# Kernel tuning notes

Hardware: AMD Instinct MI355X
Metric: run time of the kernel (lower is better)

The kernel has to match this reference:

```python
import jax, jax.numpy as jnp
import numpy as np

N = 100000       # nodes
E = 1600000      # edges per graph
D_IN, D_H, D_OUT = 256, 64, 32
TEM = (0.9, 0.8)  # tem[0], tem[1]


def setup_inputs() -> dict:
    key = jax.random.key(0)
    ks = jax.random.split(key, 17)
    f32 = jnp.float32
    return {
        "features": jax.random.normal(ks[0], (N, D_IN), f32),
        # GraphConv layer1: glorot-ish weight [in, out] + bias
        "W1": jax.random.normal(ks[1], (D_IN, D_H), f32) / np.sqrt(D_IN).astype(np.float32),
        "b1": jnp.zeros((D_H,), f32),
        "W2": jax.random.normal(ks[2], (D_H, D_OUT), f32) / np.sqrt(D_H).astype(np.float32),
        "b2": jnp.zeros((D_OUT,), f32),
        # gating linears: nn.Linear(2*d, 1) -> weight [1, 2*d], bias [1]
        "ga11_w": jax.random.normal(ks[3], (1, 2 * D_H), f32) * 0.1,
        "ga11_b": jnp.zeros((1,), f32),
        "ga12_w": jax.random.normal(ks[4], (1, 2 * D_H), f32) * 0.1,
        "ga12_b": jnp.zeros((1,), f32),
        "ga21_w": jax.random.normal(ks[5], (1, 2 * D_OUT), f32) * 0.1,
        "ga21_b": jnp.zeros((1,), f32),
        "ga22_w": jax.random.normal(ks[6], (1, 2 * D_OUT), f32) * 0.1,
        "ga22_b": jnp.zeros((1,), f32),
        # two graphs as edge lists over the same N nodes
        "src1": jax.random.randint(ks[7], (E,), 0, N, jnp.int32),
        "dst1": jax.random.randint(ks[8], (E,), 0, N, jnp.int32),
        "src2": jax.random.randint(ks[9], (E,), 0, N, jnp.int32),
        "dst2": jax.random.randint(ks[10], (E,), 0, N, jnp.int32),
    }


def _graph_conv(feat, W, b, src, dst):
    """DGL GraphConv, norm='both': D_dst^{-1/2} A^T D_src^{-1/2} X W + b.
    in_feats > out_feats for both layers, so W is applied before aggregation."""
    ones = jnp.ones(src.shape[0], feat.dtype)
    deg_out = jnp.clip(jax.ops.segment_sum(ones, src, num_segments=N), 1.0)  # [N]
    deg_in = jnp.clip(jax.ops.segment_sum(ones, dst, num_segments=N), 1.0)   # [N]
    h = (feat * jax.lax.rsqrt(deg_out)[:, None]) @ W                          # [N, d_out]
    agg = jax.ops.segment_sum(h[src], dst, num_segments=N)                    # SpMM scatter-add
    return agg * jax.lax.rsqrt(deg_in)[:, None] + b


def _gate(xa, xb, w, b, tem):
    """Faithful to: ga = softmax(Linear(cat[xa,xb]), dim=1); diag(ga) -> ga[0,0];
    xb' = tem * diag * xb. softmax over a size-1 axis gives ones; dropout is a
    no-op in eval mode."""
    ga = jnp.concatenate([xa, xb], axis=1) @ w.T + b  # [N, 1]
    ga = jax.nn.softmax(ga, axis=1)                   # all ones ([N,1], axis of size 1)
    d = ga[0, 0]                                      # torch.diag of [N,1] -> scalar ga[0,0]
    return tem * d * xb


def reference(features, W1, b1, W2, b2, ga11_w, ga11_b, ga12_w, ga12_b,
              ga21_w, ga21_b, ga22_w, ga22_b, src1, dst1, src2, dst2):
    x11 = _graph_conv(features, W1, b1, src1, dst1)
    x12 = _graph_conv(features, W1, b1, src2, dst2)
    x12 = _gate(x11, x12, ga11_w, ga11_b, TEM[1])
    x11 = _gate(x12, x11, ga12_w, ga12_b, TEM[0])
    x1 = x11 + x12
    x21 = _graph_conv(x1, W2, b2, src1, dst1)
    x22 = _graph_conv(x1, W2, b2, src2, dst2)
    x22 = _gate(x21, x22, ga21_w, ga21_b, TEM[1])
    x21 = _gate(x22, x21, ga22_w, ga22_b, TEM[0])
    return x21 + x22
```

## Files before the change

kernel.cpp:

```cpp
#include <hip/hip_runtime.h>
#include <hip/hip_bf16.h>

#define TEM0 0.9f
#define TEM1 0.8f
#define NPB 256
#define CAP 4608
#define CHUNKE 2048
#define MAXBUCK 512

typedef __attribute__((ext_vector_type(8))) short bf16x8;
typedef __attribute__((ext_vector_type(4))) float f32x4;

static __device__ __forceinline__ short f2bf(float x) {
  union { __hip_bfloat16 h; short s; } u;
  u.h = __float2bfloat16(x);
  return u.s;
}
static __device__ __forceinline__ float bf2f(short s) {
  union { float f; unsigned u; } v;
  v.u = ((unsigned)(unsigned short)s) << 16;
  return v.f;
}

__global__ __launch_bounds__(256) void bucket_gemm(
    const int* __restrict__ src1, const int* __restrict__ dst1,
    const int* __restrict__ src2, const int* __restrict__ dst2,
    int* gcur_d, int* gcur_s,
    int* __restrict__ rawD1, int* __restrict__ rawD2,
    unsigned char* __restrict__ rawS1, unsigned char* __restrict__ rawS2,
    int E, int NCH, int NBUCK,
    const float* __restrict__ X, const short* __restrict__ Wb,
    short* __restrict__ Yb, int n)
{
  __shared__ int sd[CHUNKE];
  __shared__ int ss[CHUNKE];
  __shared__ int outD[CHUNKE];
  __shared__ int hist[MAXBUCK], strt[MAXBUCK], cur[MAXBUCK], basz[MAXBUCK];
  __shared__ int tmp[256];
  __shared__ short bucketOf[CHUNKE];

  if ((int)blockIdx.x < 2 * NCH) {
    int g = 0, cb = blockIdx.x;
    if (cb >= NCH) { g = 1; cb -= NCH; }
    const int* src = g ? src2 : src1;
    const int* dst = g ? dst2 : dst1;
    int* rawD = g ? rawD2 : rawD1;
    unsigned char* rawS = g ? rawS2 : rawS1;
    int* curD = gcur_d + g * NBUCK;
    int* curS = gcur_s + g * NBUCK;
    int tid = threadIdx.x;
    int e0 = cb * CHUNKE;
    int K = min(CHUNKE, E - e0);

    for (int i = tid; i < K; i += 256) { sd[i] = dst[e0 + i]; ss[i] = src[e0 + i]; }
    hist[tid] = 0; hist[tid + 256] = 0;
    __syncthreads();

    for (int i = tid; i < K; i += 256) atomicAdd(&hist[sd[i] >> 8], 1);
    __syncthreads();
    int h0 = hist[2 * tid], h1 = hist[2 * tid + 1];
    tmp[tid] = h0 + h1;
    __syncthreads();
    for (int off = 1; off < 256; off <<= 1) {
      int t = (tid >= off) ? tmp[tid - off] : 0;
      __syncthreads();
      tmp[tid] += t;
      __syncthreads();
    }
    int ep = tmp[tid] - (h0 + h1);
    strt[2 * tid] = ep; strt[2 * tid + 1] = ep + h0;
    cur[2 * tid] = 0;  cur[2 * tid + 1] = 0;
    __syncthreads();
    for (int b = tid; b < NBUCK; b += 256) {
      int c = hist[b];
      basz[b] = c ? atomicAdd(&curD[b], c) : 0;
      int st = strt[b];
      for (int j = 0; j < c; ++j) bucketOf[st + j] = (short)b;
    }
    __syncthreads();
    for (int i = tid; i < K; i += 256) {
      int d = sd[i];
      int b = d >> 8;
      int p = atomicAdd(&cur[b], 1);
      outD[strt[b] + p] = ((d & 255) << 17) | ss[i];
    }
    __syncthreads();
    for (int i = tid; i < K; i += 256) {
      int b = bucketOf[i];
      int off = basz[b] + (i - strt[b]);
      if (off < CAP) rawD[(size_t)b * CAP + off] = outD[i];
    }

    __syncthreads();
    hist[tid] = 0; hist[tid + 256] = 0;
    __syncthreads();
    for (int i = tid; i < K; i += 256) atomicAdd(&hist[ss[i] >> 8], 1);
    __syncthreads();
    h0 = hist[2 * tid]; h1 = hist[2 * tid + 1];
    tmp[tid] = h0 + h1;
    __syncthreads();
    for (int off = 1; off < 256; off <<= 1) {
      int t = (tid >= off) ? tmp[tid - off] : 0;
      __syncthreads();
      tmp[tid] += t;
      __syncthreads();
    }
    ep = tmp[tid] - (h0 + h1);
    strt[2 * tid] = ep; strt[2 * tid + 1] = ep + h0;
    cur[2 * tid] = 0;  cur[2 * tid + 1] = 0;
    __syncthreads();
    for (int b = tid; b < NBUCK; b += 256) {
      int c = hist[b];
      basz[b] = c ? atomicAdd(&curS[b], c) : 0;
      int st = strt[b];
      for (int j = 0; j < c; ++j) bucketOf[st + j] = (short)b;
    }
    __syncthreads();
    unsigned char* outS = (unsigned char*)outD;
    for (int i = tid; i < K; i += 256) {
      int s = ss[i];
      int b = s >> 8;
      int p = atomicAdd(&cur[b], 1);
      outS[strt[b] + p] = (unsigned char)(s & 255);
    }
    __syncthreads();
    for (int i = tid; i < K; i += 256) {
      int b = bucketOf[i];
      int off = basz[b] + (i - strt[b]);
      if (off < CAP) rawS[(size_t)b * CAP + off] = outS[i];
    }
  } else {
    int bid = (int)blockIdx.x - 2 * NCH;
    int w = threadIdx.x >> 6;
    int l = threadIdx.x & 63;
    int row = bid * 64 + w * 16 + (l & 15);
    int rowc = row < n ? row : n - 1;
    int ko = (l >> 4) << 3;

    f32x4 acc[4] = {};
    const float* xrow = X + (size_t)rowc * 256;

#pragma unroll
    for (int kk = 0; kk < 8; ++kk) {
      const float4* p = reinterpret_cast<const float4*>(xrow + kk * 32 + ko);
      float4 a0 = p[0], a1 = p[1];
      bf16x8 af;
      af[0] = f2bf(a0.x); af[1] = f2bf(a0.y); af[2] = f2bf(a0.z); af[3] = f2bf(a0.w);
      af[4] = f2bf(a1.x); af[5] = f2bf(a1.y); af[6] = f2bf(a1.z); af[7] = f2bf(a1.w);
#pragma unroll
      for (int ct = 0; ct < 4; ++ct) {
        bf16x8 bfrag = *reinterpret_cast<const bf16x8*>(Wb + ((size_t)(ct * 8 + kk) * 64 + l) * 8);
        acc[ct] = __builtin_amdgcn_mfma_f32_16x16x32_bf16(af, bfrag, acc[ct], 0, 0, 0);
      }
    }

    int r0 = bid * 64 + w * 16 + ((l >> 4) << 2);
    int c0 = l & 15;
#pragma unroll
    for (int ct = 0; ct < 4; ++ct) {
#pragma unroll
      for (int i = 0; i < 4; ++i) {
        int r = r0 + i;
        if (r < n) Yb[(size_t)r * 64 + ct * 16 + c0] = f2bf(acc[ct][i]);
      }
    }
  }
}

__global__ __launch_bounds__(256) void hist_src(
    const int* __restrict__ gcur_s,
    const unsigned char* __restrict__ rawS1, const unsigned char* __restrict__ rawS2,
    int* __restrict__ co1, int* __restrict__ co2, int NBUCK, int N)
{
  __shared__ int hist[NPB];
  int g = 0, b = blockIdx.x;
  if (b >= NBUCK) { g = 1; b -= NBUCK; }
  const unsigned char* raw = (g ? rawS2 : rawS1) + (size_t)b * CAP;
  int* co = g ? co2 : co1;
  int K = gcur_s[g * NBUCK + b]; if (K > CAP) K = CAP;
  int tid = threadIdx.x;
  hist[tid] = 0;
  __syncthreads();
  for (int j = tid; j < K; j += 256) atomicAdd(&hist[raw[j]], 1);
  __syncthreads();
  int node = b * NPB + tid;
  if (node < N) co[node] = hist[tid];
}

__global__ __launch_bounds__(256) void sort_dst(
    const int* __restrict__ gcur_d,
    const int* __restrict__ rawD1, const int* __restrict__ rawD2,
    int* __restrict__ sorted1, int* __restrict__ sorted2,
    float* __restrict__ cf1, float* __restrict__ cf2,
    const int* __restrict__ co1, const int* __restrict__ co2,
    int* __restrict__ ci1, int* __restrict__ ci2,
    int* __restrict__ ns1, int* __restrict__ ns2, int NBUCK, int N)
{
  __shared__ int hist[NPB], tmp[NPB], strt[NPB], cur[NPB];
  __shared__ int sl[CAP];
  int g = 0, b = blockIdx.x;
  if (b >= NBUCK) { g = 1; b -= NBUCK; }
  const int* raw = (g ? rawD2 : rawD1) + (size_t)b * CAP;
  int* sorted = g ? sorted2 : sorted1;
  float* cf = g ? cf2 : cf1;
  const int* co = g ? co2 : co1;
  const float tem = g ? TEM1 : TEM0;
  int* ci = g ? ci2 : ci1;
  int* ns = g ? ns2 : ns1;
  int K = gcur_d[g * NBUCK + b]; if (K > CAP) K = CAP;
  int tid = threadIdx.x;

  hist[tid] = 0;
  __syncthreads();
  for (int j = tid; j < K; j += 256) atomicAdd(&hist[raw[j] >> 17], 1);
  __syncthreads();
  tmp[tid] = hist[tid];
  __syncthreads();
  for (int off = 1; off < NPB; off <<= 1) {
    int t = (tid >= off) ? tmp[tid - off] : 0;
    __syncthreads();
    tmp[tid] += t;
    __syncthreads();
  }
  strt[tid] = tmp[tid] - hist[tid];
  cur[tid] = 0;
  __syncthreads();
  for (int j = tid; j < K; j += 256) {
    int v = raw[j];
    int dl = v >> 17;
    int p = atomicAdd(&cur[dl], 1);
    sl[strt[dl] + p] = v & 0x1FFFF;
  }
  __syncthreads();
  size_t gbase = (size_t)b * CAP;
  for (int j = tid; j < K; j += 256) {
    int s = sl[j];
    sorted[gbase + j] = s;
    cf[gbase + j] = tem * rsqrtf((float)co[s]);
  }
  int node = b * NPB + tid;
  if (node < N) { ci[node] = hist[tid]; ns[node] = (int)gbase + strt[tid]; }
}

__global__ __launch_bounds__(256) void prep_w1(
    const float* __restrict__ W, short* __restrict__ Wb)
{
  int t = blockIdx.x * 256 + threadIdx.x;
  if (t >= 2048) return;
  int lane = t & 63;
  int kk = (t >> 6) & 7;
  int ct = t >> 9;
  int col = ct * 16 + (lane & 15);
  int k0 = kk * 32 + ((lane >> 4) << 3);
#pragma unroll
  for (int i = 0; i < 8; ++i)
    Wb[(size_t)t * 8 + i] = f2bf(W[(size_t)(k0 + i) * 64 + col]);
}

template<int DIN, int DOUT, int R>
__global__ __launch_bounds__(256) void gemm_rm_bf(
    const float* __restrict__ X, const float* __restrict__ W,
    short* __restrict__ Yb, int n)
{
  __shared__ float Wl[DIN * DOUT];
  for (int i = threadIdx.x; i < DIN * DOUT; i += 256) Wl[i] = W[i];
  __syncthreads();

  const int col = threadIdx.x % DOUT;
  const int rg  = threadIdx.x / DOUT;
  const int rows_per_block = (256 / DOUT) * R;
  const int row0 = blockIdx.x * rows_per_block + rg * R;

  float acc[R];
#pragma unroll
  for (int r = 0; r < R; ++r) acc[r] = 0.f;

  const float4* X4 = reinterpret_cast<const float4*>(X);

  if (row0 + R <= n) {
    for (int k4 = 0; k4 < DIN / 4; ++k4) {
      float w0 = Wl[(4 * k4 + 0) * DOUT + col];
      float w1 = Wl[(4 * k4 + 1) * DOUT + col];
      float w2 = Wl[(4 * k4 + 2) * DOUT + col];
      float w3 = Wl[(4 * k4 + 3) * DOUT + col];
#pragma unroll
      for (int r = 0; r < R; ++r) {
        float4 x = X4[(size_t)(row0 + r) * (DIN / 4) + k4];
        acc[r] = fmaf(x.x, w0, fmaf(x.y, w1, fmaf(x.z, w2, fmaf(x.w, w3, acc[r]))));
      }
    }
#pragma unroll
    for (int r = 0; r < R; ++r)
      Yb[(size_t)(row0 + r) * DOUT + col] = f2bf(acc[r]);
  } else {
    for (int k4 = 0; k4 < DIN / 4; ++k4) {
      float w0 = Wl[(4 * k4 + 0) * DOUT + col];
      float w1 = Wl[(4 * k4 + 1) * DOUT + col];
      float w2 = Wl[(4 * k4 + 2) * DOUT + col];
      float w3 = Wl[(4 * k4 + 3) * DOUT + col];
#pragma unroll
      for (int r = 0; r < R; ++r) {
        if (row0 + r < n) {
          float4 x = X4[(size_t)(row0 + r) * (DIN / 4) + k4];
          acc[r] = fmaf(x.x, w0, fmaf(x.y, w1, fmaf(x.z, w2, fmaf(x.w, w3, acc[r]))));
        }
      }
    }
    for (int r = 0; r < R; ++r)
      if (row0 + r < n) Yb[(size_t)(row0 + r) * DOUT + col] = f2bf(acc[r]);
  }
}

template<int D>
__global__ __launch_bounds__(256) void gather_nodes_bf(
    const int* __restrict__ ci1, const int* __restrict__ ns1,
    const int* __restrict__ sorted1, const float* __restrict__ cf1,
    const int* __restrict__ ci2, const int* __restrict__ ns2,
    const int* __restrict__ sorted2, const float* __restrict__ cf2,
    const short* __restrict__ Yb, const float* __restrict__ bias,
    float bscale, float* __restrict__ out, int n)
{
  constexpr int LPR = D / 8;
  constexpr int EPI = 64 / LPR;
  int wid  = (blockIdx.x * 256 + threadIdx.x) >> 6;
  int lane = threadIdx.x & 63;
  int grp = lane / LPR;
  int li  = lane % LPR;
  if (wid >= n) return;

  const bf16x8* Y8 = reinterpret_cast<const bf16x8*>(Yb);
  float a1[8], a2[8];
#pragma unroll
  for (int k = 0; k < 8; ++k) { a1[k] = 0.f; a2[k] = 0.f; }

  int len1 = ci1[wid], st1 = ns1[wid];
  int len2 = ci2[wid], st2 = ns2[wid];
  int lmax = len1 > len2 ? len1 : len2;

  for (int j = grp; j < lmax; j += EPI) {
    bool p1 = j < len1, p2 = j < len2;
    int s1 = p1 ? sorted1[st1 + j] : 0;
    int s2 = p2 ? sorted2[st2 + j] : 0;
    float c1 = p1 ? cf1[st1 + j] : 0.f;
    float c2 = p2 ? cf2[st2 + j] : 0.f;
    bf16x8 v1 = Y8[(size_t)s1 * LPR + li];
    bf16x8 v2 = Y8[(size_t)s2 * LPR + li];
#pragma unroll
    for (int k = 0; k < 8; ++k) {
      a1[k] = fmaf(c1, bf2f(v1[k]), a1[k]);
      a2[k] = fmaf(c2, bf2f(v2[k]), a2[k]);
    }
  }

  float r1 = rsqrtf((float)(len1 < 1 ? 1 : len1));
  float r2 = rsqrtf((float)(len2 < 1 ? 1 : len2));
  float acc[8];
#pragma unroll
  for (int k = 0; k < 8; ++k) acc[k] = fmaf(r1, a1[k], r2 * a2[k]);

#pragma unroll
  for (int m = LPR; m < 64; m <<= 1) {
#pragma unroll
    for (int k = 0; k < 8; ++k) acc[k] += __shfl_xor(acc[k], m);
  }

  if (grp == 0) {
    float4 b0 = reinterpret_cast<const float4*>(bias)[li * 2];
    float4 b1v = reinterpret_cast<const float4*>(bias)[li * 2 + 1];
    float4 o0, o1;
    o0.x = fmaf(bscale, b0.x, acc[0]);
    o0.y = fmaf(bscale, b0.y, acc[1]);
    o0.z = fmaf(bscale, b0.z, acc[2]);
    o0.w = fmaf(bscale, b0.w, acc[3]);
    o1.x = fmaf(bscale, b1v.x, acc[4]);
    o1.y = fmaf(bscale, b1v.y, acc[5]);
    o1.z = fmaf(bscale, b1v.z, acc[6]);
    o1.w = fmaf(bscale, b1v.w, acc[7]);
    float4* op = reinterpret_cast<float4*>(out + (size_t)wid * D + li * 8);
    op[0] = o0;
    op[1] = o1;
  }
}

extern "C" void kernel_launch(void* const* d_in, const int* in_sizes, int n_in,
                              void* d_out, int out_size, void* d_ws, size_t ws_size,
                              hipStream_t stream)
{
  const float* features = (const float*)d_in[0];
  const float* W1 = (const float*)d_in[1];
  const float* b1 = (const float*)d_in[2];
  const float* W2 = (const float*)d_in[3];
  const float* b2 = (const float*)d_in[4];
  const int* src1 = (const int*)d_in[13];
  const int* dst1 = (const int*)d_in[14];
  const int* src2 = (const int*)d_in[15];
  const int* dst2 = (const int*)d_in[16];

  const int N = in_sizes[0] / 256;
  const int E = in_sizes[13];
  const int NBUCK = (N + NPB - 1) / NPB;
  const int NCH = (E + CHUNKE - 1) / CHUNKE;

  char* ws = (char*)d_ws;
  int* gcur_d = (int*)ws;
  int* gcur_s = gcur_d + 2 * NBUCK;
  int* rawD1  = gcur_s + 2 * NBUCK;
  int* rawD2  = rawD1 + (size_t)NBUCK * CAP;
  unsigned char* rawS1 = (unsigned char*)(rawD2 + (size_t)NBUCK * CAP);
  unsigned char* rawS2 = rawS1 + (size_t)NBUCK * CAP;
  int* sorted1 = (int*)(rawS2 + (size_t)NBUCK * CAP);
  int* sorted2 = sorted1 + (size_t)NBUCK * CAP;
  float* cf1 = (float*)rawD1;
  float* cf2 = (float*)rawD2;
  int* ci1 = sorted2 + (size_t)NBUCK * CAP;
  int* ci2 = ci1 + N;
  int* ns1 = ci2 + N;
  int* ns2 = ns1 + N;
  int* co1 = ns2 + N;
  int* co2 = co1 + N;
  short* Yb = (short*)(co2 + N);
  float* x1 = (float*)(Yb + (size_t)N * 64);
  short* Wb = (short*)(x1 + (size_t)N * 64);
  float* out = (float*)d_out;

  (void)hipMemsetAsync(gcur_d, 0, (size_t)4 * NBUCK * sizeof(int), stream);
  prep_w1<<<8, 256, 0, stream>>>(W1, Wb);

  const int nbGemm = (N + 63) / 64;
  bucket_gemm<<<2 * NCH + nbGemm, 256, 0, stream>>>(
      src1, dst1, src2, dst2, gcur_d, gcur_s,
      rawD1, rawD2, rawS1, rawS2, E, NCH, NBUCK,
      features, Wb, Yb, N);

  hist_src<<<2 * NBUCK, 256, 0, stream>>>(gcur_s, rawS1, rawS2, co1, co2, NBUCK, N);
  sort_dst<<<2 * NBUCK, 256, 0, stream>>>(gcur_d, rawD1, rawD2, sorted1, sorted2,
                                          cf1, cf2, co1, co2,
                                          ci1, ci2, ns1, ns2, NBUCK, N);

  gather_nodes_bf<64><<<(N + 3) / 4, 256, 0, stream>>>(
      ci1, ns1, sorted1, cf1, ci2, ns2, sorted2, cf2,
      Yb, b1, TEM0 + TEM1, x1, N);

  gemm_rm_bf<64, 32, 8><<<(N + 63) / 64, 256, 0, stream>>>(x1, W2, Yb, N);
  gather_nodes_bf<32><<<(N + 3) / 4, 256, 0, stream>>>(
      ci1, ns1, sorted1, cf1, ci2, ns2, sorted2, cf2,
      Yb, b2, TEM0 + TEM1, out, N);
}
```

Measured before the change: 308.0 us.

## Fuse layer-1 gather with layer-2 GEMM and drop edge staging in LDS

The layer-1 neighbor aggregation now multiplies by W2 inside the same kernel. Each wavefront reduces its node's 64-wide row with shuffles and emits the 32-wide bf16 projection directly. This removes the fp32 x1 round trip through global memory and one kernel launch. Separately, the bucketing kernel no longer stages src/dst chunks in shared memory and rereads them from global instead, which cuts LDS use but adds repeated global loads. The fused kernel also loads W2 into shared memory in every block and adds a 64-step shuffle matvec per node.

```diff
diff --git a/kernel.cpp b/kernel.cpp
--- a/kernel.cpp
+++ b/kernel.cpp
@@ -32,8 +32,6 @@
     const float* __restrict__ X, const short* __restrict__ Wb,
     short* __restrict__ Yb, int n)
 {
-  __shared__ int sd[CHUNKE];
-  __shared__ int ss[CHUNKE];
   __shared__ int outD[CHUNKE];
   __shared__ int hist[MAXBUCK], strt[MAXBUCK], cur[MAXBUCK], basz[MAXBUCK];
   __shared__ int tmp[256];
@@ -52,11 +50,9 @@
     int e0 = cb * CHUNKE;
     int K = min(CHUNKE, E - e0);
 
-    for (int i = tid; i < K; i += 256) { sd[i] = dst[e0 + i]; ss[i] = src[e0 + i]; }
     hist[tid] = 0; hist[tid + 256] = 0;
     __syncthreads();
-
-    for (int i = tid; i < K; i += 256) atomicAdd(&hist[sd[i] >> 8], 1);
+    for (int i = tid; i < K; i += 256) atomicAdd(&hist[dst[e0 + i] >> 8], 1);
     __syncthreads();
     int h0 = hist[2 * tid], h1 = hist[2 * tid + 1];
     tmp[tid] = h0 + h1;
@@ -79,10 +75,10 @@
     }
     __syncthreads();
     for (int i = tid; i < K; i += 256) {
-      int d = sd[i];
+      int d = dst[e0 + i], s = src[e0 + i];
       int b = d >> 8;
       int p = atomicAdd(&cur[b], 1);
-      outD[strt[b] + p] = ((d & 255) << 17) | ss[i];
+      outD[strt[b] + p] = ((d & 255) << 17) | s;
     }
     __syncthreads();
     for (int i = tid; i < K; i += 256) {
@@ -90,11 +86,11 @@
       int off = basz[b] + (i - strt[b]);
       if (off < CAP) rawD[(size_t)b * CAP + off] = outD[i];
     }
-
-    __syncthreads();
+    __syncthreads();
+
     hist[tid] = 0; hist[tid + 256] = 0;
     __syncthreads();
-    for (int i = tid; i < K; i += 256) atomicAdd(&hist[ss[i] >> 8], 1);
+    for (int i = tid; i < K; i += 256) atomicAdd(&hist[src[e0 + i] >> 8], 1);
     __syncthreads();
     h0 = hist[2 * tid]; h1 = hist[2 * tid + 1];
     tmp[tid] = h0 + h1;
@@ -118,7 +114,7 @@
     __syncthreads();
     unsigned char* outS = (unsigned char*)outD;
     for (int i = tid; i < K; i += 256) {
-      int s = ss[i];
+      int s = src[e0 + i];
       int b = s >> 8;
       int p = atomicAdd(&cur[b], 1);
       outS[strt[b] + p] = (unsigned char)(s & 255);
@@ -257,58 +253,80 @@
     Wb[(size_t)t * 8 + i] = f2bf(W[(size_t)(k0 + i) * 64 + col]);
 }
 
-template<int DIN, int DOUT, int R>
-__global__ __launch_bounds__(256) void gemm_rm_bf(
-    const float* __restrict__ X, const float* __restrict__ W,
-    short* __restrict__ Yb, int n)
-{
-  __shared__ float Wl[DIN * DOUT];
-  for (int i = threadIdx.x; i < DIN * DOUT; i += 256) Wl[i] = W[i];
-  __syncthreads();
-
-  const int col = threadIdx.x % DOUT;
-  const int rg  = threadIdx.x / DOUT;
-  const int rows_per_block = (256 / DOUT) * R;
-  const int row0 = blockIdx.x * rows_per_block + rg * R;
-
-  float acc[R];
-#pragma unroll
-  for (int r = 0; r < R; ++r) acc[r] = 0.f;
-
-  const float4* X4 = reinterpret_cast<const float4*>(X);
-
-  if (row0 + R <= n) {
-    for (int k4 = 0; k4 < DIN / 4; ++k4) {
-      float w0 = Wl[(4 * k4 + 0) * DOUT + col];
-      float w1 = Wl[(4 * k4 + 1) * DOUT + col];
-      float w2 = Wl[(4 * k4 + 2) * DOUT + col];
-      float w3 = Wl[(4 * k4 + 3) * DOUT + col];
-#pragma unroll
-      for (int r = 0; r < R; ++r) {
-        float4 x = X4[(size_t)(row0 + r) * (DIN / 4) + k4];
-        acc[r] = fmaf(x.x, w0, fmaf(x.y, w1, fmaf(x.z, w2, fmaf(x.w, w3, acc[r]))));
-      }
-    }
-#pragma unroll
-    for (int r = 0; r < R; ++r)
-      Yb[(size_t)(row0 + r) * DOUT + col] = f2bf(acc[r]);
-  } else {
-    for (int k4 = 0; k4 < DIN / 4; ++k4) {
-      float w0 = Wl[(4 * k4 + 0) * DOUT + col];
-      float w1 = Wl[(4 * k4 + 1) * DOUT + col];
-      float w2 = Wl[(4 * k4 + 2) * DOUT + col];
-      float w3 = Wl[(4 * k4 + 3) * DOUT + col];
-#pragma unroll
-      for (int r = 0; r < R; ++r) {
-        if (row0 + r < n) {
-          float4 x = X4[(size_t)(row0 + r) * (DIN / 4) + k4];
-          acc[r] = fmaf(x.x, w0, fmaf(x.y, w1, fmaf(x.z, w2, fmaf(x.w, w3, acc[r]))));
-        }
-      }
-    }
-    for (int r = 0; r < R; ++r)
-      if (row0 + r < n) Yb[(size_t)(row0 + r) * DOUT + col] = f2bf(acc[r]);
-  }
+__global__ __launch_bounds__(256) void gather_gemm2(
+    const int* __restrict__ ci1, const int* __restrict__ ns1,
+    const int* __restrict__ sorted1, const float* __restrict__ cf1,
+    const int* __restrict__ ci2, const int* __restrict__ ns2,
+    const int* __restrict__ sorted2, const float* __restrict__ cf2,
+    const short* __restrict__ Yb, const float* __restrict__ bias,
+    float bscale, const float* __restrict__ W2,
+    short* __restrict__ Y2b, int n)
+{
+  __shared__ float W2l[64 * 32];
+  for (int i = threadIdx.x; i < 64 * 32; i += 256) W2l[i] = W2[i];
+  __syncthreads();
+
+  int wid  = (blockIdx.x * 256 + threadIdx.x) >> 6;
+  int lane = threadIdx.x & 63;
+  int grp = lane >> 3;
+  int li  = lane & 7;
+  if (wid >= n) return;
+
+  const bf16x8* Y8 = reinterpret_cast<const bf16x8*>(Yb);
+  float a1[8], a2[8];
+#pragma unroll
+  for (int k = 0; k < 8; ++k) { a1[k] = 0.f; a2[k] = 0.f; }
+
+  int len1 = ci1[wid], st1 = ns1[wid];
+  int len2 = ci2[wid], st2 = ns2[wid];
+  int lmax = len1 > len2 ? len1 : len2;
+
+  for (int j = grp; j < lmax; j += 8) {
+    bool p1 = j < len1, p2 = j < len2;
+    int s1 = p1 ? sorted1[st1 + j] : 0;
+    int s2 = p2 ? sorted2[st2 + j] : 0;
+    float c1 = p1 ? cf1[st1 + j] : 0.f;
+    float c2 = p2 ? cf2[st2 + j] : 0.f;
+    bf16x8 v1 = Y8[(size_t)s1 * 8 + li];
+    bf16x8 v2 = Y8[(size_t)s2 * 8 + li];
+#pragma unroll
+    for (int k = 0; k < 8; ++k) {
+      a1[k] = fmaf(c1, bf2f(v1[k]), a1[k]);
+      a2[k] = fmaf(c2, bf2f(v2[k]), a2[k]);
+    }
+  }
+
+  float r1 = rsqrtf((float)(len1 < 1 ? 1 : len1));
+  float r2 = rsqrtf((float)(len2 < 1 ? 1 : len2));
+  float xr[8];
+#pragma unroll
+  for (int k = 0; k < 8; ++k) xr[k] = fmaf(r1, a1[k], r2 * a2[k]);
+
+#pragma unroll
+  for (int m = 8; m < 64; m <<= 1) {
+#pragma unroll
+    for (int k = 0; k < 8; ++k) xr[k] += __shfl_xor(xr[k], m);
+  }
+
+  float4 b0 = reinterpret_cast<const float4*>(bias)[li * 2];
+  float4 b1v = reinterpret_cast<const float4*>(bias)[li * 2 + 1];
+  xr[0] = fmaf(bscale, b0.x, xr[0]);
+  xr[1] = fmaf(bscale, b0.y, xr[1]);
+  xr[2] = fmaf(bscale, b0.z, xr[2]);
+  xr[3] = fmaf(bscale, b0.w, xr[3]);
+  xr[4] = fmaf(bscale, b1v.x, xr[4]);
+  xr[5] = fmaf(bscale, b1v.y, xr[5]);
+  xr[6] = fmaf(bscale, b1v.z, xr[6]);
+  xr[7] = fmaf(bscale, b1v.w, xr[7]);
+
+  int c = lane & 31;
+  float y = 0.f;
+#pragma unroll
+  for (int k = 0; k < 64; ++k) {
+    float xk = __shfl(xr[k & 7], k >> 3);
+    y = fmaf(xk, W2l[k * 32 + c], y);
+  }
+  if (lane < 32) Y2b[(size_t)wid * 32 + c] = f2bf(y);
 }
 
 template<int D>
@@ -418,9 +436,9 @@
   int* ns2 = ns1 + N;
   int* co1 = ns2 + N;
   int* co2 = co1 + N;
-  short* Yb = (short*)(co2 + N);
-  float* x1 = (float*)(Yb + (size_t)N * 64);
-  short* Wb = (short*)(x1 + (size_t)N * 64);
+  short* Yb  = (short*)(co2 + N);
+  short* Y2b = Yb + (size_t)N * 64;
+  short* Wb  = Y2b + (size_t)N * 32;
   float* out = (float*)d_out;
 
   (void)hipMemsetAsync(gcur_d, 0, (size_t)4 * NBUCK * sizeof(int), stream);
@@ -437,12 +455,11 @@
                                           cf1, cf2, co1, co2,
                                           ci1, ci2, ns1, ns2, NBUCK, N);
 
-  gather_nodes_bf<64><<<(N + 3) / 4, 256, 0, stream>>>(
+  gather_gemm2<<<(N + 3) / 4, 256, 0, stream>>>(
       ci1, ns1, sorted1, cf1, ci2, ns2, sorted2, cf2,
-      Yb, b1, TEM0 + TEM1, x1, N);
-
-  gemm_rm_bf<64, 32, 8><<<(N + 63) / 64, 256, 0, stream>>>(x1, W2, Yb, N);
+      Yb, b1, TEM0 + TEM1, W2, Y2b, N);
+
   gather_nodes_bf<32><<<(N + 3) / 4, 256, 0, stream>>>(
       ci1, ns1, sorted1, cf1, ci2, ns2, sorted2, cf2,
-      Yb, b2, TEM0 + TEM1, out, N);
-}
+      Y2b, b2, TEM0 + TEM1, out, N);
+}
```

New measurement: 361.3 us. 1.17x slower.
